# Optimization experiments

Hardware: AMD Instinct MI355X
Metric: run time of the kernel (lower is better)

The kernel has to match this reference:

```python
import jax, jax.numpy as jnp
import numpy as np

NUM_EXPERTS = 8
TOP_K = 2
N_EMBD = 1024
B, T = 4, 2048


def setup_inputs() -> dict:
    key = jax.random.key(0)
    k_x, k_g, k_e = jax.random.split(key, 3)
    x = jax.random.normal(k_x, (B, T, N_EMBD), dtype=jnp.float32)
    # torch nn.Linear weight layout: (out_features, in_features); y = x @ W.T
    scale = 1.0 / np.sqrt(N_EMBD)
    gate_w = jax.random.uniform(k_g, (NUM_EXPERTS, N_EMBD), dtype=jnp.float32,
                                minval=-scale, maxval=scale)
    expert_w = jax.random.uniform(k_e, (NUM_EXPERTS, N_EMBD, N_EMBD), dtype=jnp.float32,
                                  minval=-scale, maxval=scale)
    return {"x": x, "gate_w": gate_w, "expert_w": expert_w}


def reference(x, gate_w, expert_w):
    Bb, Tt, C = x.shape
    xf = x.reshape(Bb * Tt, C)                        # (N, C)
    logits = xf @ gate_w.T                            # (N, E)
    w, sel = jax.lax.top_k(logits, TOP_K)             # (N, K) each
    # softmax over the selected logits in float32, cast back (matches torch)
    w = jax.nn.softmax(w.astype(jnp.float32), axis=1).astype(xf.dtype)
    # scatter per-token routing weights into a dense (N, E) combine matrix
    n = xf.shape[0]
    w_full = jnp.zeros((n, NUM_EXPERTS), dtype=xf.dtype)
    w_full = w_full.at[jnp.arange(n)[:, None], sel].add(w)
    # all-expert outputs: y_e = x @ W_e.T  -> (N, E, C)
    expert_out = jnp.einsum('nc,edc->ned', xf, expert_w)
    out = jnp.einsum('ne,ned->nd', w_full, expert_out)  # combine
    return out.reshape(Bb, Tt, C)
```

## Files before the change

### kernel.cpp

```cpp
#include <hip/hip_runtime.h>
#include <hip/hip_bf16.h>

#define NEXP 8
#define NEMB 1024
#define NTOK 8192
#define BM 256
#define BN 256
#define BK 32
#define NK  (NEMB / BK)
#define RBSLOTS 16
#define BLD_STRIPE 512

typedef __attribute__((ext_vector_type(8))) short  bf16x8;
typedef __attribute__((ext_vector_type(8))) unsigned short u16x8;
typedef __attribute__((ext_vector_type(4))) float  f32x4;

#define XB_BYTES   (NTOK * NEMB * 2)
#define WB_BYTES   (NEXP * NEMB * NEMB * 2)
#define CNT_OFF    (XB_BYTES + WB_BYTES)
#define LTOK_OFF   (CNT_OFF + 256)
#define LWT_OFF    (LTOK_OFF + NEXP * NTOK * 4)
#define SELW_OFF   (LWT_OFF + NEXP * NTOK * 4)

__device__ __forceinline__ unsigned short f2bf(float f) {
    unsigned u = __builtin_bit_cast(unsigned, f);
    unsigned r = (u + 0x7fffu + ((u >> 16) & 1u)) >> 16;
    return (unsigned short)r;
}

__global__ void k_cvt_w(const float* __restrict__ w, unsigned short* __restrict__ wb) {
    int i = (blockIdx.x * blockDim.x + threadIdx.x) * 8;
    f32x4 v0 = *reinterpret_cast<const f32x4*>(w + i);
    f32x4 v1 = *reinterpret_cast<const f32x4*>(w + i + 4);
    u16x8 o;
#pragma unroll
    for (int j = 0; j < 4; ++j) { o[j] = f2bf(v0[j]); o[4 + j] = f2bf(v1[j]); }
    *reinterpret_cast<u16x8*>(wb + i) = o;
}

__global__ __launch_bounds__(256)
void k_gate(const float* __restrict__ x, const float* __restrict__ gw,
            unsigned short* __restrict__ xb, int4* __restrict__ selw) {
    int t = threadIdx.x, wave = t >> 6, lane = t & 63;
    int n = blockIdx.x * 4 + wave;

    const float* xr = x + (size_t)n * NEMB + lane * 16;
    f32x4 xv[4];
#pragma unroll
    for (int j = 0; j < 4; ++j) xv[j] = *reinterpret_cast<const f32x4*>(xr + j * 4);

    u16x8 o0, o1;
#pragma unroll
    for (int q = 0; q < 4; ++q) {
        o0[q] = f2bf(xv[0][q]); o0[4 + q] = f2bf(xv[1][q]);
        o1[q] = f2bf(xv[2][q]); o1[4 + q] = f2bf(xv[3][q]);
    }
    u16x8* xo = reinterpret_cast<u16x8*>(xb + (size_t)n * NEMB + lane * 16);
    xo[0] = o0; xo[1] = o1;

    float p[NEXP];
#pragma unroll
    for (int e = 0; e < NEXP; ++e) {
        const float* gr = gw + e * NEMB + lane * 16;
        f32x4 a = xv[0] * *reinterpret_cast<const f32x4*>(gr);
#pragma unroll
        for (int j = 1; j < 4; ++j) a += xv[j] * *reinterpret_cast<const f32x4*>(gr + j * 4);
        p[e] = a[0] + a[1] + a[2] + a[3];
    }
#pragma unroll
    for (int e = 0; e < NEXP; ++e) {
        float v = p[e];
#pragma unroll
        for (int m = 1; m < 64; m <<= 1) v += __shfl_xor(v, m, 64);
        p[e] = v;
    }
    if (lane == 0) {
        int e0 = 0; float b0 = p[0];
#pragma unroll
        for (int e = 1; e < NEXP; ++e) if (p[e] > b0) { b0 = p[e]; e0 = e; }
        int e1 = -1; float b1 = -3.4e38f;
#pragma unroll
        for (int e = 0; e < NEXP; ++e) if (e != e0 && p[e] > b1) { b1 = p[e]; e1 = e; }
        float ex = __expf(b1 - b0);
        float inv = 1.f / (1.f + ex);
        int4 s;
        s.x = e0; s.y = e1;
        s.z = __float_as_int(inv); s.w = __float_as_int(ex * inv);
        selw[n] = s;
    }
}

__global__ __launch_bounds__(256)
void k_build(const int4* __restrict__ selw, int* __restrict__ counts,
             int* __restrict__ ltok, float* __restrict__ lwt) {
    int e = blockIdx.y;
    int n0 = blockIdx.x * BLD_STRIPE;
    __shared__ int lcnt, base;
    __shared__ int   toks[BLD_STRIPE];
    __shared__ float wts[BLD_STRIPE];
    if (threadIdx.x == 0) lcnt = 0;
    __syncthreads();
    for (int i = threadIdx.x; i < BLD_STRIPE; i += 256) {
        int4 s = selw[n0 + i];
        if (s.x == e) {
            int p = atomicAdd(&lcnt, 1);
            toks[p] = n0 + i; wts[p] = __int_as_float(s.z);
        }
        if (s.y == e) {
            int p = atomicAdd(&lcnt, 1);
            toks[p] = n0 + i; wts[p] = __int_as_float(s.w);
        }
    }
    __syncthreads();
    if (threadIdx.x == 0) base = atomicAdd(&counts[e], lcnt);
    __syncthreads();
    for (int i = threadIdx.x; i < lcnt; i += 256) {
        ltok[e * NTOK + base + i] = toks[i];
        lwt[e * NTOK + base + i]  = wts[i];
    }
}

__global__ void k_pad(const int* __restrict__ counts, int* __restrict__ ltok,
                      float* __restrict__ lwt) {
    int e = blockIdx.x;
    int c = counts[e];
    int cp = (c + BM - 1) & ~(BM - 1);
    for (int i = c + threadIdx.x; i < cp; i += blockDim.x) {
        ltok[e * NTOK + i] = -1;
        lwt[e * NTOK + i]  = 0.f;
    }
}

__global__ __launch_bounds__(512, 2)
void k_gemm(const unsigned short* __restrict__ xb, const unsigned short* __restrict__ wb,
            const int* __restrict__ counts, const int* __restrict__ ltok,
            const float* __restrict__ lwt, float* __restrict__ out) {
    int e  = blockIdx.z;
    int rb = blockIdx.y;
    int cb = blockIdx.x;
    int cnt = counts[e];
    if (rb * BM >= cnt) return;

    __shared__ unsigned short As[3][BM * BK];
    __shared__ unsigned short Bs[3][BN * BK];
    __shared__ int   tokS[BM];
    __shared__ float wS[BM];

    int t = threadIdx.x;
    int lane = t & 63, wave = t >> 6;
    int wr = wave >> 2, wc = wave & 3;

    if (t < BM) {
        tokS[t] = ltok[e * NTOK + rb * BM + t];
        wS[t]   = lwt[e * NTOK + rb * BM + t];
    }

    const unsigned short* aSrc[2];
    const unsigned short* bSrc[2];
    int ldOff[2];
#pragma unroll
    for (int i = 0; i < 2; ++i) {
        int idx = i * 512 + t;
        int r   = idx >> 2;
        int csw = (idx & 3) ^ (r & 3);
        int tok = ltok[e * NTOK + rb * BM + r];
        int tokc = tok < 0 ? 0 : tok;
        aSrc[i] = xb + (size_t)tokc * NEMB + csw * 8;
        bSrc[i] = wb + (size_t)e * NEMB * NEMB + (size_t)(cb * BN + r) * NEMB + csw * 8;
        ldOff[i] = (i * 512 + wave * 64) * 8;
    }

#define STAGE_A(dst, kk)                                                            \
    {                                                                               \
        _Pragma("unroll")                                                           \
        for (int i = 0; i < 2; ++i)                                                 \
            __builtin_amdgcn_global_load_lds(                                       \
                (const __attribute__((address_space(1))) void*)(aSrc[i] + (kk) * BK),\
                (__attribute__((address_space(3))) void*)((dst) + ldOff[i]), 16, 0, 0);\
    }
#define STAGE_B(dst, kk)                                                            \
    {                                                                               \
        _Pragma("unroll")                                                           \
        for (int i = 0; i < 2; ++i)                                                 \
            __builtin_amdgcn_global_load_lds(                                       \
                (const __attribute__((address_space(1))) void*)(bSrc[i] + (kk) * BK),\
                (__attribute__((address_space(3))) void*)((dst) + ldOff[i]), 16, 0, 0);\
    }

    f32x4 acc[8][4];
#pragma unroll
    for (int m = 0; m < 8; ++m)
#pragma unroll
        for (int n = 0; n < 4; ++n) acc[m][n] = (f32x4){0.f, 0.f, 0.f, 0.f};

    int fr = lane & 15, fq = lane >> 4;
    int ch = fq ^ (fr & 3);
    int aBase = (wr * 128 + fr) * BK + ch * 8;
    int bBase = (wc * 64  + fr) * BK + ch * 8;

    STAGE_A(&As[0][0], 0); STAGE_B(&Bs[0][0], 0);
    STAGE_A(&As[1][0], 1); STAGE_B(&Bs[1][0], 1);

    for (int tau = 0; tau < NK; ++tau) {
        const unsigned short* aCur = &As[tau % 3][0];
        const unsigned short* bCur = &Bs[tau % 3][0];
        unsigned short* aNxt = &As[(tau + 2) % 3][0];
        unsigned short* bNxt = &Bs[(tau + 2) % 3][0];

        if (tau < NK - 1) { asm volatile("s_waitcnt vmcnt(4)" ::: "memory"); }
        else              { asm volatile("s_waitcnt vmcnt(0)" ::: "memory"); }
        __builtin_amdgcn_sched_barrier(0);
        __builtin_amdgcn_s_barrier();

        bool doStage = (tau + 2) < NK;

        if (doStage) STAGE_A(aNxt, tau + 2);
        bf16x8 bfr[4], af[4];
#pragma unroll
        for (int n = 0; n < 4; ++n)
            bfr[n] = *reinterpret_cast<const bf16x8*>(bCur + bBase + n * 16 * BK);
#pragma unroll
        for (int m = 0; m < 4; ++m)
            af[m] = *reinterpret_cast<const bf16x8*>(aCur + aBase + m * 16 * BK);
        asm volatile("s_waitcnt lgkmcnt(0)" ::: "memory");
        __builtin_amdgcn_sched_barrier(0);
        __builtin_amdgcn_s_setprio(1);
#pragma unroll
        for (int m = 0; m < 4; ++m)
#pragma unroll
            for (int n = 0; n < 4; ++n)
                acc[m][n] = __builtin_amdgcn_mfma_f32_16x16x32_bf16(
                    af[m], bfr[n], acc[m][n], 0, 0, 0);
        __builtin_amdgcn_s_setprio(0);

        if (doStage) STAGE_B(bNxt, tau + 2);
#pragma unroll
        for (int m = 0; m < 4; ++m)
            af[m] = *reinterpret_cast<const bf16x8*>(aCur + aBase + (m + 4) * 16 * BK);
        asm volatile("s_waitcnt lgkmcnt(0)" ::: "memory");
        __builtin_amdgcn_sched_barrier(0);
        __builtin_amdgcn_s_setprio(1);
#pragma unroll
        for (int m = 0; m < 4; ++m)
#pragma unroll
            for (int n = 0; n < 4; ++n)
                acc[m + 4][n] = __builtin_amdgcn_mfma_f32_16x16x32_bf16(
                    af[m], bfr[n], acc[m + 4][n], 0, 0, 0);
        __builtin_amdgcn_s_setprio(0);
    }
#undef STAGE_A
#undef STAGE_B

#pragma unroll
    for (int m = 0; m < 8; ++m) {
#pragma unroll
        for (int jj = 0; jj < 4; ++jj) {
            int row = wr * 128 + m * 16 + fq * 4 + jj;
            int tok = tokS[row];
            if (tok < 0) continue;
            float wgt = wS[row];
            float* orow = out + (size_t)tok * NEMB + cb * BN + wc * 64 + fr;
#pragma unroll
            for (int n = 0; n < 4; ++n)
                unsafeAtomicAdd(orow + n * 16, wgt * acc[m][n][jj]);
        }
    }
}

extern "C" void kernel_launch(void* const* d_in, const int* in_sizes, int n_in,
                              void* d_out, int out_size, void* d_ws, size_t ws_size,
                              hipStream_t stream) {
    const float* x  = (const float*)d_in[0];
    const float* gw = (const float*)d_in[1];
    const float* ew = (const float*)d_in[2];
    float* out = (float*)d_out;

    char* ws = (char*)d_ws;
    unsigned short* xb = (unsigned short*)(ws);
    unsigned short* wb = (unsigned short*)(ws + XB_BYTES);
    int*   counts = (int*)(ws + CNT_OFF);
    int*   ltok   = (int*)(ws + LTOK_OFF);
    float* lwt    = (float*)(ws + LWT_OFF);
    int4*  selw   = (int4*)(ws + SELW_OFF);

    hipMemsetAsync(counts, 0, 8 * sizeof(int), stream);
    hipMemsetAsync(out, 0, (size_t)NTOK * NEMB * sizeof(float), stream);

    k_cvt_w<<<4096, 256, 0, stream>>>(ew, wb);
    k_gate<<<NTOK / 4, 256, 0, stream>>>(x, gw, xb, selw);
    k_build<<<dim3(NTOK / BLD_STRIPE, NEXP), 256, 0, stream>>>(selw, counts, ltok, lwt);
    k_pad<<<8, 128, 0, stream>>>(counts, ltok, lwt);
    k_gemm<<<dim3(NEMB / BN, RBSLOTS, NEXP), 512, 0, stream>>>(xb, wb, counts, ltok, lwt, out);
}
```

Measured before the change: 160.5 us.

## Restructure grouped GEMM into BK=64 double-buffered, 8-phase interleaved pipeline

```diff
diff --git a/kernel.cpp b/kernel.cpp
--- a/kernel.cpp
+++ b/kernel.cpp
@@ -6,9 +6,9 @@
 #define NTOK 8192
 #define BM 256
 #define BN 256
-#define BK 32
+#define BK 64
 #define NK  (NEMB / BK)
-#define RBSLOTS 16
+#define NIT (NK / 2)
 #define BLD_STRIPE 512
 
 typedef __attribute__((ext_vector_type(8))) short  bf16x8;
@@ -138,54 +138,72 @@
     int e  = blockIdx.z;
     int rb = blockIdx.y;
     int cb = blockIdx.x;
-    int cnt = counts[e];
-    if (rb * BM >= cnt) return;
-
-    __shared__ unsigned short As[3][BM * BK];
-    __shared__ unsigned short Bs[3][BN * BK];
+    if (rb * BM >= counts[e]) return;
+
+    __shared__ unsigned short As[2][BM * BK];
+    __shared__ unsigned short Bs[2][BN * BK];
     __shared__ int   tokS[BM];
     __shared__ float wS[BM];
 
-    int t = threadIdx.x;
-    int lane = t & 63, wave = t >> 6;
+    int t = threadIdx.x, lane = t & 63, wave = t >> 6;
     int wr = wave >> 2, wc = wave & 3;
+    int fr = lane & 15, fq = lane >> 4, fs = fr & 7;
+    int pk0 = fq ^ fs, pk1 = (fq + 4) ^ fs;
 
     if (t < BM) {
         tokS[t] = ltok[e * NTOK + rb * BM + t];
         wS[t]   = lwt[e * NTOK + rb * BM + t];
     }
 
-    const unsigned short* aSrc[2];
-    const unsigned short* bSrc[2];
-    int ldOff[2];
-#pragma unroll
-    for (int i = 0; i < 2; ++i) {
-        int idx = i * 512 + t;
-        int r   = idx >> 2;
-        int csw = (idx & 3) ^ (r & 3);
-        int tok = ltok[e * NTOK + rb * BM + r];
+    int c0 = t & 7, r0 = t >> 3;
+    int csw = c0 ^ (r0 & 7);
+    const unsigned short* aS[4];
+    const unsigned short* bS[4];
+#pragma unroll
+    for (int j = 0; j < 4; ++j) {
+        int row = j * 64 + r0;
+        int tok = ltok[e * NTOK + rb * BM + row];
         int tokc = tok < 0 ? 0 : tok;
-        aSrc[i] = xb + (size_t)tokc * NEMB + csw * 8;
-        bSrc[i] = wb + (size_t)e * NEMB * NEMB + (size_t)(cb * BN + r) * NEMB + csw * 8;
-        ldOff[i] = (i * 512 + wave * 64) * 8;
-    }
-
-#define STAGE_A(dst, kk)                                                            \
-    {                                                                               \
-        _Pragma("unroll")                                                           \
-        for (int i = 0; i < 2; ++i)                                                 \
-            __builtin_amdgcn_global_load_lds(                                       \
-                (const __attribute__((address_space(1))) void*)(aSrc[i] + (kk) * BK),\
-                (__attribute__((address_space(3))) void*)((dst) + ldOff[i]), 16, 0, 0);\
-    }
-#define STAGE_B(dst, kk)                                                            \
-    {                                                                               \
-        _Pragma("unroll")                                                           \
-        for (int i = 0; i < 2; ++i)                                                 \
-            __builtin_amdgcn_global_load_lds(                                       \
-                (const __attribute__((address_space(1))) void*)(bSrc[i] + (kk) * BK),\
-                (__attribute__((address_space(3))) void*)((dst) + ldOff[i]), 16, 0, 0);\
-    }
+        aS[j] = xb + (size_t)tokc * NEMB + csw * 8;
+        bS[j] = wb + (size_t)e * NEMB * NEMB + (size_t)(cb * BN + row) * NEMB + csw * 8;
+    }
+    int off0 = wave * 512;
+    int off1 = 4096 + wave * 512;
+
+#define GLL(src, dst)                                                                \
+    __builtin_amdgcn_global_load_lds(                                                \
+        (const __attribute__((address_space(1))) void*)(src),                        \
+        (__attribute__((address_space(3))) void*)(dst), 16, 0, 0)
+#define STG_A(buf, h, kt) if ((kt) < NK) {                                           \
+    GLL(aS[(h)*2 + 0] + (kt)*BK, &As[buf][(h)*8192 + off0]);                         \
+    GLL(aS[(h)*2 + 1] + (kt)*BK, &As[buf][(h)*8192 + off1]); }
+#define STG_B(buf, h, kt) if ((kt) < NK) {                                           \
+    GLL(bS[(h)*2 + 0] + (kt)*BK, &Bs[buf][(h)*8192 + off0]);                         \
+    GLL(bS[(h)*2 + 1] + (kt)*BK, &Bs[buf][(h)*8192 + off1]); }
+
+#define LDA(mh, buf) { _Pragma("unroll")                                             \
+    for (int m = 0; m < 4; ++m) {                                                    \
+        int row = ((mh)*4 + m)*32 + wr*16 + fr;                                      \
+        af[m][0] = *reinterpret_cast<const bf16x8*>(&As[buf][row*BK + pk0*8]);       \
+        af[m][1] = *reinterpret_cast<const bf16x8*>(&As[buf][row*BK + pk1*8]); } }
+#define LDB(dst, nh, buf) { _Pragma("unroll")                                        \
+    for (int n = 0; n < 2; ++n) {                                                    \
+        int row = ((nh)*2 + n)*64 + wc*16 + fr;                                      \
+        dst[n][0] = *reinterpret_cast<const bf16x8*>(&Bs[buf][row*BK + pk0*8]);      \
+        dst[n][1] = *reinterpret_cast<const bf16x8*>(&Bs[buf][row*BK + pk1*8]); } }
+#define MM(mh, nh, bfx) { _Pragma("unroll")                                          \
+    for (int m = 0; m < 4; ++m) { _Pragma("unroll")                                  \
+        for (int n = 0; n < 2; ++n) {                                                \
+            acc[(mh)*4+m][(nh)*2+n] = __builtin_amdgcn_mfma_f32_16x16x32_bf16(       \
+                af[m][0], bfx[n][0], acc[(mh)*4+m][(nh)*2+n], 0, 0, 0);              \
+            acc[(mh)*4+m][(nh)*2+n] = __builtin_amdgcn_mfma_f32_16x16x32_bf16(       \
+                af[m][1], bfx[n][1], acc[(mh)*4+m][(nh)*2+n], 0, 0, 0); } } }
+#define BAR   __builtin_amdgcn_s_barrier()
+#define LGKM0 asm volatile("s_waitcnt lgkmcnt(0)" ::: "memory")
+#define VM6   asm volatile("s_waitcnt vmcnt(6)" ::: "memory")
+#define VM0   asm volatile("s_waitcnt vmcnt(0)" ::: "memory")
+#define PRI1  __builtin_amdgcn_s_setprio(1)
+#define PRI0  __builtin_amdgcn_s_setprio(0)
 
     f32x4 acc[8][4];
 #pragma unroll
@@ -193,76 +211,63 @@
 #pragma unroll
         for (int n = 0; n < 4; ++n) acc[m][n] = (f32x4){0.f, 0.f, 0.f, 0.f};
 
-    int fr = lane & 15, fq = lane >> 4;
-    int ch = fq ^ (fr & 3);
-    int aBase = (wr * 128 + fr) * BK + ch * 8;
-    int bBase = (wc * 64  + fr) * BK + ch * 8;
-
-    STAGE_A(&As[0][0], 0); STAGE_B(&Bs[0][0], 0);
-    STAGE_A(&As[1][0], 1); STAGE_B(&Bs[1][0], 1);
-
-    for (int tau = 0; tau < NK; ++tau) {
-        const unsigned short* aCur = &As[tau % 3][0];
-        const unsigned short* bCur = &Bs[tau % 3][0];
-        unsigned short* aNxt = &As[(tau + 2) % 3][0];
-        unsigned short* bNxt = &Bs[(tau + 2) % 3][0];
-
-        if (tau < NK - 1) { asm volatile("s_waitcnt vmcnt(4)" ::: "memory"); }
-        else              { asm volatile("s_waitcnt vmcnt(0)" ::: "memory"); }
-        __builtin_amdgcn_sched_barrier(0);
-        __builtin_amdgcn_s_barrier();
-
-        bool doStage = (tau + 2) < NK;
-
-        if (doStage) STAGE_A(aNxt, tau + 2);
-        bf16x8 bfr[4], af[4];
-#pragma unroll
-        for (int n = 0; n < 4; ++n)
-            bfr[n] = *reinterpret_cast<const bf16x8*>(bCur + bBase + n * 16 * BK);
-#pragma unroll
-        for (int m = 0; m < 4; ++m)
-            af[m] = *reinterpret_cast<const bf16x8*>(aCur + aBase + m * 16 * BK);
-        asm volatile("s_waitcnt lgkmcnt(0)" ::: "memory");
-        __builtin_amdgcn_sched_barrier(0);
-        __builtin_amdgcn_s_setprio(1);
-#pragma unroll
-        for (int m = 0; m < 4; ++m)
-#pragma unroll
-            for (int n = 0; n < 4; ++n)
-                acc[m][n] = __builtin_amdgcn_mfma_f32_16x16x32_bf16(
-                    af[m], bfr[n], acc[m][n], 0, 0, 0);
-        __builtin_amdgcn_s_setprio(0);
-
-        if (doStage) STAGE_B(bNxt, tau + 2);
-#pragma unroll
-        for (int m = 0; m < 4; ++m)
-            af[m] = *reinterpret_cast<const bf16x8*>(aCur + aBase + (m + 4) * 16 * BK);
-        asm volatile("s_waitcnt lgkmcnt(0)" ::: "memory");
-        __builtin_amdgcn_sched_barrier(0);
-        __builtin_amdgcn_s_setprio(1);
-#pragma unroll
-        for (int m = 0; m < 4; ++m)
-#pragma unroll
-            for (int n = 0; n < 4; ++n)
-                acc[m + 4][n] = __builtin_amdgcn_mfma_f32_16x16x32_bf16(
-                    af[m], bfr[n], acc[m + 4][n], 0, 0, 0);
-        __builtin_amdgcn_s_setprio(0);
-    }
-#undef STAGE_A
-#undef STAGE_B
+    bf16x8 af[4][2], bf0[2][2], bf1[2][2];
+
+    STG_A(0, 0, 0); STG_B(0, 0, 0); STG_A(0, 1, 0); STG_B(0, 1, 0);
+    STG_A(1, 0, 1); STG_B(1, 0, 1); STG_B(1, 1, 1);
+    VM6; LGKM0; BAR;
+
+    for (int i = 0; i < NIT; ++i) {
+        int kt1 = 2 * i + 1;
+        int n0  = 2 * i + 2;
+        int n1  = 2 * i + 3;
+        bool lastIt = (i == NIT - 1);
+
+        LDA(0, 0); LDB(bf0, 0, 0);
+        STG_A(1, 1, kt1);
+        BAR; LGKM0; PRI1; MM(0, 0, bf0); PRI0; BAR;
+        LDB(bf1, 1, 0);
+        STG_A(0, 0, n0);
+        BAR; LGKM0; PRI1; MM(0, 1, bf1); PRI0; BAR;
+        LDA(1, 0);
+        STG_B(0, 0, n0);
+        BAR; LGKM0; PRI1; MM(1, 0, bf0); PRI0; BAR;
+        STG_A(0, 1, n0);
+        if (lastIt) { VM0; } else { VM6; }
+        BAR; PRI1; MM(1, 1, bf1); PRI0; BAR;
+        LDA(0, 1); LDB(bf0, 0, 1);
+        STG_B(0, 1, n0);
+        BAR; LGKM0; PRI1; MM(0, 0, bf0); PRI0; BAR;
+        LDB(bf1, 1, 1);
+        STG_A(1, 0, n1);
+        BAR; LGKM0; PRI1; MM(0, 1, bf1); PRI0; BAR;
+        LDA(1, 1);
+        STG_B(1, 0, n1);
+        BAR; LGKM0; PRI1; MM(1, 0, bf0); PRI0; BAR;
+        STG_B(1, 1, n1);
+        if (!lastIt) { VM6; }
+        BAR; PRI1; MM(1, 1, bf1); PRI0; BAR;
+    }
+
+#undef GLL
+#undef STG_A
+#undef STG_B
+#undef LDA
+#undef LDB
+#undef MM
 
 #pragma unroll
     for (int m = 0; m < 8; ++m) {
 #pragma unroll
         for (int jj = 0; jj < 4; ++jj) {
-            int row = wr * 128 + m * 16 + fq * 4 + jj;
+            int row = m * 32 + wr * 16 + fq * 4 + jj;
             int tok = tokS[row];
             if (tok < 0) continue;
             float wgt = wS[row];
-            float* orow = out + (size_t)tok * NEMB + cb * BN + wc * 64 + fr;
+            float* orow = out + (size_t)tok * NEMB + cb * BN + wc * 16 + fr;
 #pragma unroll
             for (int n = 0; n < 4; ++n)
-                unsafeAtomicAdd(orow + n * 16, wgt * acc[m][n][jj]);
+                unsafeAtomicAdd(orow + n * 64, wgt * acc[m][n][jj]);
         }
     }
 }
@@ -290,5 +295,5 @@
     k_gate<<<NTOK / 4, 256, 0, stream>>>(x, gw, xb, selw);
     k_build<<<dim3(NTOK / BLD_STRIPE, NEXP), 256, 0, stream>>>(selw, counts, ltok, lwt);
     k_pad<<<8, 128, 0, stream>>>(counts, ltok, lwt);
-    k_gemm<<<dim3(NEMB / BN, RBSLOTS, NEXP), 512, 0, stream>>>(xb, wb, counts, ltok, lwt, out);
-}
+    k_gemm<<<dim3(NEMB / BN, 16, NEXP), 512, 0, stream>>>(xb, wb, counts, ltok, lwt, out);
+}
```

After: 146.4 us. -8.8%, faster.
